# Kernel optimization log

Measured on AMD Instinct MI355X. Metric: run time of the kernel, lower is better.

The kernel has to match this reference:

```python
import jax, jax.numpy as jnp
import numpy as np

HIDDEN = 896
NUM_Q_HEADS = 14
NUM_KV_HEADS = 2
HEAD_DIM = 64
ROPE_BASE = 10000.0
B, S = 4, 2048


def rotate_half(x):
    x1, x2 = jnp.split(x, 2, axis=-1)
    return jnp.concatenate((-x2, x1), axis=-1)


def rope_cos_sin(position_ids):
    # position_ids: [B, S] int -> cos/sin [B, 1, S, HEAD_DIM]
    inv_freq = 1.0 / (ROPE_BASE ** (jnp.arange(0, HEAD_DIM, 2, dtype=jnp.float32) / HEAD_DIM))
    freqs = position_ids.astype(jnp.float32)[..., None] * inv_freq  # [B,S,D/2]
    emb = jnp.concatenate((freqs, freqs), axis=-1)  # [B,S,D]
    return jnp.cos(emb)[:, None, :, :], jnp.sin(emb)[:, None, :, :]


def setup_inputs() -> dict:
    key = jax.random.key(0)
    k1, k2, k3, k4, k5 = jax.random.split(key, 5)
    s = 1.0 / np.sqrt(HIDDEN)
    return {
        "hidden_states": jax.random.normal(k1, (B, S, HIDDEN), dtype=jnp.float32),
        "position_ids": jnp.broadcast_to(jnp.arange(S, dtype=jnp.int64), (B, S)),
        "Wq": jax.random.normal(k2, (HIDDEN, NUM_Q_HEADS * HEAD_DIM), dtype=jnp.float32) * s,
        "Wk": jax.random.normal(k3, (HIDDEN, NUM_KV_HEADS * HEAD_DIM), dtype=jnp.float32) * s,
        "Wv": jax.random.normal(k4, (HIDDEN, NUM_KV_HEADS * HEAD_DIM), dtype=jnp.float32) * s,
        "Wo": jax.random.normal(k5, (NUM_Q_HEADS * HEAD_DIM, HIDDEN), dtype=jnp.float32) * s,
    }


def reference(hidden_states, position_ids, Wq, Wk, Wv, Wo):
    b, s, _ = hidden_states.shape
    n_rep = NUM_Q_HEADS // NUM_KV_HEADS

    q = (hidden_states @ Wq).reshape(b, s, NUM_Q_HEADS, HEAD_DIM).transpose(0, 2, 1, 3)   # [B,Hq,S,D]
    k = (hidden_states @ Wk).reshape(b, s, NUM_KV_HEADS, HEAD_DIM).transpose(0, 2, 1, 3)  # [B,Hkv,S,D]
    v = (hidden_states @ Wv).reshape(b, s, NUM_KV_HEADS, HEAD_DIM).transpose(0, 2, 1, 3)

    cos, sin = rope_cos_sin(position_ids)  # [B,1,S,D]
    q = q * cos + rotate_half(q) * sin
    k = k * cos + rotate_half(k) * sin

    # repeat_interleave KV heads to match query heads
    k = jnp.repeat(k, n_rep, axis=1)  # [B,Hq,S,D]
    v = jnp.repeat(v, n_rep, axis=1)

    scale = 1.0 / jnp.sqrt(jnp.float32(HEAD_DIM))
    attn = jnp.einsum('bhqd,bhkd->bhqk', q, k) * scale  # [B,Hq,S,S]
    attn = jax.nn.softmax(attn, axis=-1)
    out = jnp.einsum('bhqk,bhkd->bhqd', attn, v)  # [B,Hq,S,D]
    out = out.transpose(0, 2, 1, 3).reshape(b, s, NUM_Q_HEADS * HEAD_DIM)
    return out @ Wo
```

## Files before the change

### kernel.cpp

```cpp
#include <hip/hip_runtime.h>
#include <hip/hip_bf16.h>
#include <math.h>

typedef unsigned short ushort_t;
typedef __bf16 bf16x8 __attribute__((ext_vector_type(8)));
typedef float f32x4 __attribute__((ext_vector_type(4)));

#define HIDDEN 896
#define NQH 14
#define NKVH 2
#define HD 64
#define SEQ 2048
#define NBATCH 4

__device__ inline ushort_t f2bf(float x) {
  union { float f; unsigned u; } c; c.f = x;
  unsigned r = c.u + 0x7FFFu + ((c.u >> 16) & 1u);
  return (ushort_t)(r >> 16);
}

__device__ inline unsigned pack2bf(float a, float b) {
  union { float f; unsigned u; } ca, cb; ca.f = a; cb.f = b;
  unsigned ua = ca.u + 0x8000u, ub = cb.u + 0x8000u;
  return __builtin_amdgcn_perm(ub, ua, 0x07060302);
}

__device__ inline bf16x8 ldfrag(const ushort_t* p) {
  return *reinterpret_cast<const bf16x8*>(p);
}

__device__ inline void async16(const ushort_t* g, ushort_t* l) {
  __builtin_amdgcn_global_load_lds(
      (const __attribute__((address_space(1))) void*)g,
      (__attribute__((address_space(3))) void*)l, 16, 0, 0);
}


__device__ inline void transpose_sec(const float* __restrict__ in, ushort_t* __restrict__ out,
                                     int K, int N, int bx, int by) {
  __shared__ float tile[32][33];
  int k0 = by * 32, n0 = bx * 32;
  for (int r = threadIdx.y; r < 32; r += 8) {
    int k = k0 + r, n = n0 + threadIdx.x;
    tile[r][threadIdx.x] = (k < K && n < N) ? in[(size_t)k * N + n] : 0.f;
  }
  __syncthreads();
  for (int r = threadIdx.y; r < 32; r += 8) {
    int n = n0 + r, k = k0 + threadIdx.x;
    if (n < N && k < K) out[(size_t)n * K + k] = f2bf(tile[threadIdx.x][r]);
  }
}

__global__ void k_prep(const float* __restrict__ hidden, ushort_t* __restrict__ hb,
                       const float* __restrict__ Wq, const float* __restrict__ Wk,
                       const float* __restrict__ Wv, const float* __restrict__ Wo,
                       ushort_t* __restrict__ wT, ushort_t* __restrict__ woT,
                       float2* __restrict__ ctab) {
  const int blk = blockIdx.x;
  const int tid = threadIdx.y * 32 + threadIdx.x;
  if (blk < 7168) {
    int i = blk * 256 + tid;
    float4 v = reinterpret_cast<const float4*>(hidden)[i];
    ushort4 o;
    o.x = f2bf(v.x); o.y = f2bf(v.y); o.z = f2bf(v.z); o.w = f2bf(v.w);
    reinterpret_cast<ushort4*>(hb)[i] = o;
  } else if (blk < 7424) {
    int idx = (blk - 7168) * 256 + tid;
    int s = idx >> 5, dp = idx & 31;
    float inv = exp2f(-(float)dp * 0.41524101186092596f);
    float ang = (float)s * inv;
    float sn, cn;
    sincosf(ang, &sn, &cn);
    ctab[idx] = make_float2(cn, sn);
  } else if (blk < 8208) {
    int t = blk - 7424;
    transpose_sec(Wq, wT, 896, 896, t % 28, t / 28);
  } else if (blk < 8320) {
    int t = blk - 8208;
    transpose_sec(Wk, wT + (size_t)896 * 896, 896, 128, t % 4, t / 4);
  } else if (blk < 8432) {
    int t = blk - 8320;
    transpose_sec(Wv, wT + (size_t)1024 * 896, 896, 128, t % 4, t / 4);
  } else {
    int t = blk - 8432;
    transpose_sec(Wo, woT, 896, 896, t % 28, t / 28);
  }
}

__global__ __launch_bounds__(256) void k_qkv(
    const ushort_t* __restrict__ hb,
    const ushort_t* __restrict__ wT,
    const int* __restrict__ pos_ids,
    const float2* __restrict__ ctab,
    ushort_t* __restrict__ Qg,
    ushort_t* __restrict__ Kg,
    ushort_t* __restrict__ Vtg) {
  __shared__ ushort_t smem[12288];
  ushort_t* sa = smem;
  ushort_t* sbb = smem + 4096;

  const int f = blockIdx.x;
  const int x = f & 7, s8 = f >> 3;
  const int sect = s8 % 9;
  const int mt = (s8 / 9) * 8 + x;
  const int nt0 = sect * 128;
  const int m0 = mt * 64;
  const int tid = threadIdx.x;
  const int wave = tid >> 6, lane = tid & 63;
  const int l15 = lane & 15, quad = lane >> 4;
  const int wm = wave >> 1, wn = wave & 1;
  const int sw = l15 & 7;

  f32x4 acc[2][4];
  const f32x4 z4 = {0.f, 0.f, 0.f, 0.f};
#pragma unroll
  for (int a = 0; a < 2; ++a)
#pragma unroll
    for (int b = 0; b < 4; ++b) acc[a][b] = z4;

  for (int kt = 0; kt < 14; ++kt) {
    const int k0 = kt * 64;
    __syncthreads();
#pragma unroll
    for (int i = 0; i < 2; ++i) {
      int id = i * 256 + tid;
      int row = id >> 3;
      int cs = (id & 7) ^ (row & 7);
      async16(hb + (size_t)(m0 + row) * HIDDEN + k0 + cs * 8, sa + (i * 256 + wave * 64) * 8);
    }
#pragma unroll
    for (int i = 0; i < 4; ++i) {
      int id = i * 256 + tid;
      int row = id >> 3;
      int cs = (id & 7) ^ (row & 7);
      async16(wT + (size_t)(nt0 + row) * HIDDEN + k0 + cs * 8, sbb + (i * 256 + wave * 64) * 8);
    }
    __syncthreads();
    bf16x8 af[2][2], bf[4][2];
#pragma unroll
    for (int kc = 0; kc < 2; ++kc) {
      int c = kc * 4 + quad;
#pragma unroll
      for (int mb = 0; mb < 2; ++mb)
        af[mb][kc] = ldfrag(sa + ((wm * 32 + mb * 16 + l15) * 8 + (c ^ sw)) * 8);
#pragma unroll
      for (int nb = 0; nb < 4; ++nb)
        bf[nb][kc] = ldfrag(sbb + ((wn * 64 + nb * 16 + l15) * 8 + (c ^ sw)) * 8);
    }
#pragma unroll
    for (int mb = 0; mb < 2; ++mb)
#pragma unroll
      for (int nb = 0; nb < 4; ++nb) {
        acc[mb][nb] = __builtin_amdgcn_mfma_f32_16x16x32_bf16(af[mb][0], bf[nb][0], acc[mb][nb], 0, 0, 0);
        acc[mb][nb] = __builtin_amdgcn_mfma_f32_16x16x32_bf16(af[mb][1], bf[nb][1], acc[mb][nb], 0, 0, 0);
      }
  }

  if (sect < 8) {
    const bool isQ = sect < 7;
    const float csc = isQ ? 0.125f * 1.4426950408889634f : 1.0f;
    ushort_t* dst = isQ ? Qg : Kg;
    const int nheads = isQ ? NQH : NKVH;
    const int hh = isQ ? sect * 2 + wn : wn;
#pragma unroll
    for (int mb = 0; mb < 2; ++mb)
#pragma unroll
      for (int r = 0; r < 4; ++r) {
        int token = m0 + wm * 32 + mb * 16 + quad * 4 + r;
        int b = token >> 11, s = token & 2047;
        int pos = pos_ids[token];
        size_t base = ((size_t)(b * nheads + hh) * SEQ + s) * HD;
#pragma unroll
        for (int nb = 0; nb < 2; ++nb) {
          float2 cs = ctab[pos * 32 + nb * 16 + l15];
          float x0 = acc[mb][nb][r];
          float x1 = acc[mb][nb + 2][r];
          float y0 = (x0 * cs.x - x1 * cs.y) * csc;
          float y1 = (x1 * cs.x + x0 * cs.y) * csc;
          dst[base + nb * 16 + l15]      = f2bf(y0);
          dst[base + nb * 16 + l15 + 32] = f2bf(y1);
        }
      }
  } else {
    __syncthreads();
    ushort_t* vt = smem;
#pragma unroll
    for (int mb = 0; mb < 2; ++mb) {
      int tl = wm * 32 + mb * 16 + quad * 4;
      int chunk = tl >> 3, ofs = tl & 7;
#pragma unroll
      for (int nb = 0; nb < 4; ++nb) {
        int row = wn * 64 + nb * 16 + l15;
        int slot = chunk ^ (row & 7);
        ushort_t* p = vt + row * 64 + slot * 8 + ofs;
        *reinterpret_cast<unsigned*>(p)     = pack2bf(acc[mb][nb][0], acc[mb][nb][1]);
        *reinterpret_cast<unsigned*>(p + 2) = pack2bf(acc[mb][nb][2], acc[mb][nb][3]);
      }
    }
    __syncthreads();
    const int bb = m0 >> 11, s0 = m0 & 2047;
#pragma unroll
    for (int i = 0; i < 4; ++i) {
      int id = i * 256 + tid;
      int row = id >> 3, ch = id & 7;
      int kvh = row >> 6, d = row & 63;
      int slot = ch ^ (row & 7);
      uint4 v = *reinterpret_cast<const uint4*>(vt + row * 64 + slot * 8);
      *reinterpret_cast<uint4*>(Vtg + ((size_t)(bb * NKVH + kvh) * HD + d) * SEQ + s0 + ch * 8) = v;
    }
  }
}

__global__ __launch_bounds__(128, 2) void k_attn(
    const ushort_t* __restrict__ Qg,
    const ushort_t* __restrict__ Kg,
    const ushort_t* __restrict__ Vtg,
    ushort_t* __restrict__ attn) {
  __shared__ ushort_t pbuf[2][64 * 72];
  __shared__ float lbuf[64];

  const int f = blockIdx.x;
  const int x = f & 7, s8 = f >> 3;
  const int lh = s8 % 7;
  const int qc = s8 / 7;
  const int b = x >> 1, kvh = x & 1;
  const int h = kvh * 7 + lh;
  const int bh = b * NQH + h;
  const int tid = threadIdx.x;
  const int wave = tid >> 6, lane = tid & 63;
  const int l15 = lane & 15, quad = lane >> 4;
  const int q0 = qc * 64;
  ushort_t* pw = pbuf[wave];

  bf16x8 qf[4][2];
#pragma unroll
  for (int qs = 0; qs < 4; ++qs) {
    const size_t qb = ((size_t)bh * SEQ + q0 + qs * 16 + l15) * HD + quad * 8;
    qf[qs][0] = ldfrag(Qg + qb);
    qf[qs][1] = ldfrag(Qg + qb + 32);
  }

  bf16x8 ones;
#pragma unroll
  for (int i = 0; i < 8; ++i) ones[i] = (__bf16)1.0f;

  const ushort_t* Kb = Kg + (size_t)(b * NKVH + kvh) * SEQ * HD;
  const ushort_t* Vb = Vtg + (size_t)(b * NKVH + kvh) * HD * SEQ;

  f32x4 o[4][4];
  f32x4 lfr[4];
  const f32x4 z4 = {0.f, 0.f, 0.f, 0.f};
#pragma unroll
  for (int qs = 0; qs < 4; ++qs) {
    lfr[qs] = z4;
#pragma unroll
    for (int nb = 0; nb < 4; ++nb) o[qs][nb] = z4;
  }

  for (int jt = 0; jt < 16; ++jt) {
    const int s0 = (jt * 2 + wave) * 64;

#pragma unroll
    for (int nb = 0; nb < 4; ++nb) {
      const ushort_t* kr = Kb + (size_t)(s0 + nb * 16 + l15) * HD + quad * 8;
      bf16x8 kf0 = ldfrag(kr);
      bf16x8 kf1 = ldfrag(kr + 32);
#pragma unroll
      for (int qs = 0; qs < 4; ++qs) {
        f32x4 t = z4;
        t = __builtin_amdgcn_mfma_f32_16x16x32_bf16(kf0, qf[qs][0], t, 0, 0, 0);
        t = __builtin_amdgcn_mfma_f32_16x16x32_bf16(kf1, qf[qs][1], t, 0, 0, 0);
        float p0 = __builtin_amdgcn_exp2f(t[0]);
        float p1 = __builtin_amdgcn_exp2f(t[1]);
        float p2 = __builtin_amdgcn_exp2f(t[2]);
        float p3 = __builtin_amdgcn_exp2f(t[3]);
        uint2 d;
        d.x = pack2bf(p0, p1);
        d.y = pack2bf(p2, p3);
        *reinterpret_cast<uint2*>(pw + (qs * 16 + l15) * 72 + nb * 16 + quad * 4) = d;
      }
    }

    bf16x8 pf[4][2];
#pragma unroll
    for (int qs = 0; qs < 4; ++qs) {
      pf[qs][0] = ldfrag(pw + (qs * 16 + l15) * 72 + quad * 8);
      pf[qs][1] = ldfrag(pw + (qs * 16 + l15) * 72 + 32 + quad * 8);
      lfr[qs] = __builtin_amdgcn_mfma_f32_16x16x32_bf16(pf[qs][0], ones, lfr[qs], 0, 0, 0);
      lfr[qs] = __builtin_amdgcn_mfma_f32_16x16x32_bf16(pf[qs][1], ones, lfr[qs], 0, 0, 0);
    }

#pragma unroll
    for (int nb = 0; nb < 4; ++nb) {
      const ushort_t* vr = Vb + (size_t)(nb * 16 + l15) * SEQ + s0 + quad * 8;
      bf16x8 vf0 = ldfrag(vr);
      bf16x8 vf1 = ldfrag(vr + 32);
#pragma unroll
      for (int qs = 0; qs < 4; ++qs) {
        o[qs][nb] = __builtin_amdgcn_mfma_f32_16x16x32_bf16(pf[qs][0], vf0, o[qs][nb], 0, 0, 0);
        o[qs][nb] = __builtin_amdgcn_mfma_f32_16x16x32_bf16(pf[qs][1], vf1, o[qs][nb], 0, 0, 0);
      }
    }
  }

  float* fb = reinterpret_cast<float*>(pbuf[1]);
  if (wave == 1) {
#pragma unroll
    for (int qs = 0; qs < 4; ++qs)
#pragma unroll
      for (int r = 0; r < 4; ++r) {
        int q = qs * 16 + quad * 4 + r;
        fb[q * 33 + l15]      = o[qs][0][r];
        fb[q * 33 + 16 + l15] = o[qs][1][r];
        if (l15 == 0) lbuf[q] = lfr[qs][r];
      }
  }
  __syncthreads();
  if (wave == 0) {
#pragma unroll
    for (int qs = 0; qs < 4; ++qs)
#pragma unroll
      for (int r = 0; r < 4; ++r) {
        int q = qs * 16 + quad * 4 + r;
        o[qs][0][r] += fb[q * 33 + l15];
        o[qs][1][r] += fb[q * 33 + 16 + l15];
        lfr[qs][r] += lbuf[q];
      }
  }
  __syncthreads();
  if (wave == 1) {
#pragma unroll
    for (int qs = 0; qs < 4; ++qs)
#pragma unroll
      for (int r = 0; r < 4; ++r) {
        int q = qs * 16 + quad * 4 + r;
        fb[q * 33 + l15]      = o[qs][2][r];
        fb[q * 33 + 16 + l15] = o[qs][3][r];
      }
  }
  __syncthreads();
  if (wave == 0) {
#pragma unroll
    for (int qs = 0; qs < 4; ++qs)
#pragma unroll
      for (int r = 0; r < 4; ++r) {
        int q = qs * 16 + quad * 4 + r;
        o[qs][2][r] += fb[q * 33 + l15];
        o[qs][3][r] += fb[q * 33 + 16 + l15];
      }
#pragma unroll
    for (int qs = 0; qs < 4; ++qs)
#pragma unroll
      for (int r = 0; r < 4; ++r) {
        float inv = 1.0f / lfr[qs][r];
        int qg = q0 + qs * 16 + quad * 4 + r;
#pragma unroll
        for (int nb = 0; nb < 4; ++nb) {
          float val = o[qs][nb][r] * inv;
          attn[(size_t)(b * SEQ + qg) * (NQH * HD) + h * HD + nb * 16 + l15] = f2bf(val);
        }
      }
  }
}

__global__ __launch_bounds__(256) void k_oproj(
    const ushort_t* __restrict__ attn,
    const ushort_t* __restrict__ woT,
    float* __restrict__ out) {
  __shared__ ushort_t smem[12288];
  ushort_t* sa = smem;
  ushort_t* sbb = smem + 4096;

  const int f = blockIdx.x;
  const int x = f & 7, s8 = f >> 3;
  const int n_sect = s8 % 7;
  const int mt = (s8 / 7) * 8 + x;
  const int n0 = n_sect * 128;
  const int m0 = mt * 64;
  const int tid = threadIdx.x;
  const int wave = tid >> 6, lane = tid & 63;
  const int l15 = lane & 15, quad = lane >> 4;
  const int wm = wave >> 1, wn = wave & 1;
  const int sw = l15 & 7;

  f32x4 acc[2][4];
  const f32x4 z4 = {0.f, 0.f, 0.f, 0.f};
#pragma unroll
  for (int a = 0; a < 2; ++a)
#pragma unroll
    for (int b = 0; b < 4; ++b) acc[a][b] = z4;

  for (int kt = 0; kt < 14; ++kt) {
    const int k0 = kt * 64;
    __syncthreads();
#pragma unroll
    for (int i = 0; i < 2; ++i) {
      int id = i * 256 + tid;
      int row = id >> 3;
      int cs = (id & 7) ^ (row & 7);
      async16(attn + (size_t)(m0 + row) * HIDDEN + k0 + cs * 8, sa + (i * 256 + wave * 64) * 8);
    }
#pragma unroll
    for (int i = 0; i < 4; ++i) {
      int id = i * 256 + tid;
      int row = id >> 3;
      int cs = (id & 7) ^ (row & 7);
      async16(woT + (size_t)(n0 + row) * HIDDEN + k0 + cs * 8, sbb + (i * 256 + wave * 64) * 8);
    }
    __syncthreads();
    bf16x8 af[2][2], bf[4][2];
#pragma unroll
    for (int kc = 0; kc < 2; ++kc) {
      int c = kc * 4 + quad;
#pragma unroll
      for (int mb = 0; mb < 2; ++mb)
        af[mb][kc] = ldfrag(sa + ((wm * 32 + mb * 16 + l15) * 8 + (c ^ sw)) * 8);
#pragma unroll
      for (int nb = 0; nb < 4; ++nb)
        bf[nb][kc] = ldfrag(sbb + ((wn * 64 + nb * 16 + l15) * 8 + (c ^ sw)) * 8);
    }
#pragma unroll
    for (int mb = 0; mb < 2; ++mb)
#pragma unroll
      for (int nb = 0; nb < 4; ++nb) {
        acc[mb][nb] = __builtin_amdgcn_mfma_f32_16x16x32_bf16(af[mb][0], bf[nb][0], acc[mb][nb], 0, 0, 0);
        acc[mb][nb] = __builtin_amdgcn_mfma_f32_16x16x32_bf16(af[mb][1], bf[nb][1], acc[mb][nb], 0, 0, 0);
      }
  }

#pragma unroll
  for (int mb = 0; mb < 2; ++mb)
#pragma unroll
    for (int nb = 0; nb < 4; ++nb)
#pragma unroll
      for (int r = 0; r < 4; ++r)
        out[(size_t)(m0 + wm * 32 + mb * 16 + quad * 4 + r) * HIDDEN +
            n0 + wn * 64 + nb * 16 + l15] = acc[mb][nb][r];
}


extern "C" void kernel_launch(void* const* d_in, const int* in_sizes, int n_in,
                              void* d_out, int out_size, void* d_ws, size_t ws_size,
                              hipStream_t stream) {
  (void)in_sizes; (void)n_in; (void)out_size; (void)ws_size;
  const float* hidden = (const float*)d_in[0];
  const int* pos      = (const int*)d_in[1];
  const float* Wq     = (const float*)d_in[2];
  const float* Wk     = (const float*)d_in[3];
  const float* Wv     = (const float*)d_in[4];
  const float* Wo     = (const float*)d_in[5];
  float* out = (float*)d_out;

  char* ws = (char*)d_ws;
  ushort_t* hb   = (ushort_t*)(ws);
  ushort_t* wT   = (ushort_t*)(ws + 14680064);
  float2*   ctab = (float2*)  (ws + 16744448);
  ushort_t* Qg   = (ushort_t*)(ws + 17268736);
  ushort_t* Kg   = (ushort_t*)(ws + 31948800);
  ushort_t* Vtg  = (ushort_t*)(ws + 34045952);
  ushort_t* attn = (ushort_t*)(ws + 36143104);
  ushort_t* woT  = (ushort_t*)(ws + 50823168);

  k_prep<<<9216, dim3(32, 8), 0, stream>>>(hidden, hb, Wq, Wk, Wv, Wo, wT, woT, ctab);
  k_qkv<<<1152, 256, 0, stream>>>(hb, wT, pos, ctab, Qg, Kg, Vtg);
  k_attn<<<1792, 128, 0, stream>>>(Qg, Kg, Vtg, attn);
  k_oproj<<<896, 256, 0, stream>>>(attn, woT, out);
}
```

Measured before the change: 259.4 us.

## Restructure attention to share LDS-staged K/V tiles across four query-split waves

```diff
diff --git a/kernel.cpp b/kernel.cpp
--- a/kernel.cpp
+++ b/kernel.cpp
@@ -211,62 +211,72 @@
   }
 }
 
-__global__ __launch_bounds__(128, 2) void k_attn(
+__global__ __launch_bounds__(256) void k_attn(
     const ushort_t* __restrict__ Qg,
     const ushort_t* __restrict__ Kg,
     const ushort_t* __restrict__ Vtg,
     ushort_t* __restrict__ attn) {
-  __shared__ ushort_t pbuf[2][64 * 72];
-  __shared__ float lbuf[64];
+  __shared__ ushort_t kbuf[64 * 64];
+  __shared__ ushort_t vbuf[64 * 64];
+  __shared__ ushort_t pbuf[4][32 * 72];
 
   const int f = blockIdx.x;
   const int x = f & 7, s8 = f >> 3;
   const int lh = s8 % 7;
-  const int qc = s8 / 7;
+  const int qt = s8 / 7;
   const int b = x >> 1, kvh = x & 1;
   const int h = kvh * 7 + lh;
   const int bh = b * NQH + h;
   const int tid = threadIdx.x;
   const int wave = tid >> 6, lane = tid & 63;
   const int l15 = lane & 15, quad = lane >> 4;
-  const int q0 = qc * 64;
-  ushort_t* pw = pbuf[wave];
-
-  bf16x8 qf[4][2];
-#pragma unroll
-  for (int qs = 0; qs < 4; ++qs) {
-    const size_t qb = ((size_t)bh * SEQ + q0 + qs * 16 + l15) * HD + quad * 8;
+  const int q0 = qt * 128;
+
+  bf16x8 qf[2][2];
+#pragma unroll
+  for (int qs = 0; qs < 2; ++qs) {
+    const size_t qb = ((size_t)bh * SEQ + q0 + wave * 32 + qs * 16 + l15) * HD + quad * 8;
     qf[qs][0] = ldfrag(Qg + qb);
     qf[qs][1] = ldfrag(Qg + qb + 32);
   }
 
-  bf16x8 ones;
-#pragma unroll
-  for (int i = 0; i < 8; ++i) ones[i] = (__bf16)1.0f;
-
-  const ushort_t* Kb = Kg + (size_t)(b * NKVH + kvh) * SEQ * HD;
-  const ushort_t* Vb = Vtg + (size_t)(b * NKVH + kvh) * HD * SEQ;
-
-  f32x4 o[4][4];
-  f32x4 lfr[4];
+  const size_t kbase = (size_t)(b * NKVH + kvh) * SEQ * HD;
+  const size_t vbase = (size_t)(b * NKVH + kvh) * HD * SEQ;
+
+  const int srow = tid >> 3;
+  const int sc0 = (tid & 7) ^ (srow & 7);
+  const int srow2 = (256 + tid) >> 3;
+  const int sc2 = (tid & 7) ^ (srow2 & 7);
+  const int sbase1 = wave * 64 * 8;
+  const int sbase2 = (256 + wave * 64) * 8;
+
+  float l_part[2] = {0.f, 0.f};
+  f32x4 o[2][4];
   const f32x4 z4 = {0.f, 0.f, 0.f, 0.f};
 #pragma unroll
-  for (int qs = 0; qs < 4; ++qs) {
-    lfr[qs] = z4;
+  for (int qs = 0; qs < 2; ++qs)
 #pragma unroll
     for (int nb = 0; nb < 4; ++nb) o[qs][nb] = z4;
-  }
-
-  for (int jt = 0; jt < 16; ++jt) {
-    const int s0 = (jt * 2 + wave) * 64;
+
+  ushort_t* pw = pbuf[wave];
+
+  for (int jt = 0; jt < 32; ++jt) {
+    const int s0 = jt * 64;
+    __syncthreads();
+    async16(Kg + kbase + (size_t)(s0 + srow) * HD + sc0 * 8, kbuf + sbase1);
+    async16(Vtg + vbase + (size_t)srow * SEQ + s0 + sc0 * 8, vbuf + sbase1);
+    async16(Kg + kbase + (size_t)(s0 + srow2) * HD + sc2 * 8, kbuf + sbase2);
+    async16(Vtg + vbase + (size_t)srow2 * SEQ + s0 + sc2 * 8, vbuf + sbase2);
+    __syncthreads();
 
 #pragma unroll
     for (int nb = 0; nb < 4; ++nb) {
-      const ushort_t* kr = Kb + (size_t)(s0 + nb * 16 + l15) * HD + quad * 8;
-      bf16x8 kf0 = ldfrag(kr);
-      bf16x8 kf1 = ldfrag(kr + 32);
-#pragma unroll
-      for (int qs = 0; qs < 4; ++qs) {
+      int row = nb * 16 + l15;
+      int sw = row & 7;
+      bf16x8 kf0 = ldfrag(kbuf + (row * 8 + (quad ^ sw)) * 8);
+      bf16x8 kf1 = ldfrag(kbuf + (row * 8 + ((4 + quad) ^ sw)) * 8);
+#pragma unroll
+      for (int qs = 0; qs < 2; ++qs) {
         f32x4 t = z4;
         t = __builtin_amdgcn_mfma_f32_16x16x32_bf16(kf0, qf[qs][0], t, 0, 0, 0);
         t = __builtin_amdgcn_mfma_f32_16x16x32_bf16(kf1, qf[qs][1], t, 0, 0, 0);
@@ -274,6 +284,7 @@
         float p1 = __builtin_amdgcn_exp2f(t[1]);
         float p2 = __builtin_amdgcn_exp2f(t[2]);
         float p3 = __builtin_amdgcn_exp2f(t[3]);
+        l_part[qs] += (p0 + p1) + (p2 + p3);
         uint2 d;
         d.x = pack2bf(p0, p1);
         d.y = pack2bf(p2, p3);
@@ -281,85 +292,47 @@
       }
     }
 
-    bf16x8 pf[4][2];
-#pragma unroll
-    for (int qs = 0; qs < 4; ++qs) {
+    bf16x8 pf[2][2];
+#pragma unroll
+    for (int qs = 0; qs < 2; ++qs) {
       pf[qs][0] = ldfrag(pw + (qs * 16 + l15) * 72 + quad * 8);
       pf[qs][1] = ldfrag(pw + (qs * 16 + l15) * 72 + 32 + quad * 8);
-      lfr[qs] = __builtin_amdgcn_mfma_f32_16x16x32_bf16(pf[qs][0], ones, lfr[qs], 0, 0, 0);
-      lfr[qs] = __builtin_amdgcn_mfma_f32_16x16x32_bf16(pf[qs][1], ones, lfr[qs], 0, 0, 0);
-    }
-
+    }
 #pragma unroll
     for (int nb = 0; nb < 4; ++nb) {
-      const ushort_t* vr = Vb + (size_t)(nb * 16 + l15) * SEQ + s0 + quad * 8;
-      bf16x8 vf0 = ldfrag(vr);
-      bf16x8 vf1 = ldfrag(vr + 32);
-#pragma unroll
-      for (int qs = 0; qs < 4; ++qs) {
+      int row = nb * 16 + l15;
+      int sw = row & 7;
+      bf16x8 vf0 = ldfrag(vbuf + (row * 8 + (quad ^ sw)) * 8);
+      bf16x8 vf1 = ldfrag(vbuf + (row * 8 + ((4 + quad) ^ sw)) * 8);
+#pragma unroll
+      for (int qs = 0; qs < 2; ++qs) {
         o[qs][nb] = __builtin_amdgcn_mfma_f32_16x16x32_bf16(pf[qs][0], vf0, o[qs][nb], 0, 0, 0);
         o[qs][nb] = __builtin_amdgcn_mfma_f32_16x16x32_bf16(pf[qs][1], vf1, o[qs][nb], 0, 0, 0);
       }
     }
   }
 
-  float* fb = reinterpret_cast<float*>(pbuf[1]);
-  if (wave == 1) {
-#pragma unroll
-    for (int qs = 0; qs < 4; ++qs)
-#pragma unroll
-      for (int r = 0; r < 4; ++r) {
-        int q = qs * 16 + quad * 4 + r;
-        fb[q * 33 + l15]      = o[qs][0][r];
-        fb[q * 33 + 16 + l15] = o[qs][1][r];
-        if (l15 == 0) lbuf[q] = lfr[qs][r];
-      }
-  }
-  __syncthreads();
-  if (wave == 0) {
-#pragma unroll
-    for (int qs = 0; qs < 4; ++qs)
-#pragma unroll
-      for (int r = 0; r < 4; ++r) {
-        int q = qs * 16 + quad * 4 + r;
-        o[qs][0][r] += fb[q * 33 + l15];
-        o[qs][1][r] += fb[q * 33 + 16 + l15];
-        lfr[qs][r] += lbuf[q];
-      }
-  }
-  __syncthreads();
-  if (wave == 1) {
-#pragma unroll
-    for (int qs = 0; qs < 4; ++qs)
-#pragma unroll
-      for (int r = 0; r < 4; ++r) {
-        int q = qs * 16 + quad * 4 + r;
-        fb[q * 33 + l15]      = o[qs][2][r];
-        fb[q * 33 + 16 + l15] = o[qs][3][r];
-      }
-  }
-  __syncthreads();
-  if (wave == 0) {
-#pragma unroll
-    for (int qs = 0; qs < 4; ++qs)
-#pragma unroll
-      for (int r = 0; r < 4; ++r) {
-        int q = qs * 16 + quad * 4 + r;
-        o[qs][2][r] += fb[q * 33 + l15];
-        o[qs][3][r] += fb[q * 33 + 16 + l15];
-      }
-#pragma unroll
-    for (int qs = 0; qs < 4; ++qs)
-#pragma unroll
-      for (int r = 0; r < 4; ++r) {
-        float inv = 1.0f / lfr[qs][r];
-        int qg = q0 + qs * 16 + quad * 4 + r;
-#pragma unroll
-        for (int nb = 0; nb < 4; ++nb) {
-          float val = o[qs][nb][r] * inv;
-          attn[(size_t)(b * SEQ + qg) * (NQH * HD) + h * HD + nb * 16 + l15] = f2bf(val);
-        }
-      }
+#pragma unroll
+  for (int qs = 0; qs < 2; ++qs) {
+    float s = l_part[qs];
+    s += __shfl_xor(s, 16);
+    s += __shfl_xor(s, 32);
+    l_part[qs] = s;
+  }
+
+#pragma unroll
+  for (int qs = 0; qs < 2; ++qs) {
+    float il = 1.0f / l_part[qs];
+#pragma unroll
+    for (int r = 0; r < 4; ++r) {
+      float inv = __shfl(il, quad * 4 + r);
+      int qg = q0 + wave * 32 + qs * 16 + quad * 4 + r;
+#pragma unroll
+      for (int nb = 0; nb < 4; ++nb) {
+        float val = o[qs][nb][r] * inv;
+        attn[(size_t)(b * SEQ + qg) * (NQH * HD) + h * HD + nb * 16 + l15] = f2bf(val);
+      }
+    }
   }
 }
 
@@ -463,6 +436,6 @@
 
   k_prep<<<9216, dim3(32, 8), 0, stream>>>(hidden, hb, Wq, Wk, Wv, Wo, wT, woT, ctab);
   k_qkv<<<1152, 256, 0, stream>>>(hb, wT, pos, ctab, Qg, Kg, Vtg);
-  k_attn<<<1792, 128, 0, stream>>>(Qg, Kg, Vtg, attn);
+  k_attn<<<896, 256, 0, stream>>>(Qg, Kg, Vtg, attn);
   k_oproj<<<896, 256, 0, stream>>>(attn, woT, out);
 }
```

New measurement: 229.0 us. 1.13x faster.
